# Kernel tuning notes

Measured on AMD Instinct MI355X. Metric: run time of the kernel, lower is better.

The kernel has to match this reference:

```python
import jax, jax.numpy as jnp
import numpy as np

B = 256      # batch
ZD = 128     # z_dim
HIN = 128    # H_inputs
H = 512      # hidden
HT = 32      # H_t
N = 16384    # num nodes
RW = 16      # rw_len
TEMP = 1.0
P_DROP = 0.2
EPS_C = 0.1  # constraints epsilon


def setup_inputs() -> dict:
    key = jax.random.key(0)
    ks = jax.random.split(key, 20)
    def w(k, shape, fan):
        return (jax.random.normal(k, shape, jnp.float32) / np.float32(np.sqrt(fan)))
    z = lambda n: jnp.zeros((n,), jnp.float32)
    u = jax.random.uniform(ks[14], (RW, B, N), jnp.float32)
    return {
        "latent": jax.random.normal(ks[0], (B, ZD + 1), jnp.float32),
        "inputs0": jnp.zeros((B, HIN), jnp.float32),
        "Wc": w(ks[1], (ZD, ZD + 1), ZD + 1), "bc": z(ZD),
        "Ws": w(ks[2], (H, ZD), ZD), "bs": z(H),
        "Wh": w(ks[3], (H, H), H), "bh": z(H),
        "Wcc": w(ks[4], (H, H), H), "bcc": z(H),
        "W_ih": w(ks[5], (4 * H, HIN), HIN), "b_ih": z(4 * H),
        "W_hh": w(ks[6], (4 * H, H), H), "b_hh": z(4 * H),
        "W_up": w(ks[7], (N, H), H), "b_up": z(N),
        "W_down": w(ks[8], (HIN, N), N),
        "Wt_down": w(ks[9], (HT, H), H), "bt_down": z(HT),
        "Wt_pred": w(ks[10], (1, HT), HT),
        "Wt_up": w(ks[11], (HT, 1), 1), "bt_up": z(HT),
        "W_vt": w(ks[12], (HIN, HIN + HT), HIN + HT),
        "W_prob": w(ks[13], (1, HIN), HIN),
        # pre-sampled Gumbel noise per step (torch.rand -> gumbel)
        "gumbel": -jnp.log(-jnp.log(u + 1e-20) + 1e-20),
        # uniforms for dropout masks in TimeDecoder (forced train mode)
        "drop_u": jax.random.uniform(ks[15], (RW, B, HT), jnp.float32),
    }


def reference(latent, inputs0, Wc, bc, Ws, bs, Wh, bh, Wcc, bcc,
              W_ih, b_ih, W_hh, b_hh, W_up, b_up, W_down,
              Wt_down, bt_down, Wt_pred, Wt_up, bt_up, W_vt, W_prob,
              gumbel, drop_u):
    # induced=True path: compress latent, init (h, c)
    lat = jnp.tanh(latent @ Wc.T + bc)               # [B, ZD]
    s = jnp.tanh(lat @ Ws.T + bs)                    # [B, H]
    h0 = jnp.tanh(s @ Wh.T + bh)
    c0 = jnp.tanh(s @ Wcc.T + bcc)
    keep = 1.0 - P_DROP

    def step(carry, xs):
        x, h, c, last_t = carry
        g, du = xs
        # torch LSTMCell: gate order i, f, g, o
        gates = x @ W_ih.T + b_ih + h @ W_hh.T + b_hh  # [B, 4H]
        i, f, gg, o = jnp.split(gates, 4, axis=1)
        c2 = jax.nn.sigmoid(f) * c + jax.nn.sigmoid(i) * jnp.tanh(gg)
        h2 = jax.nn.sigmoid(o) * jnp.tanh(c2)
        # node logits + gumbel-softmax sample
        p = h2 @ W_up.T + b_up                         # [B, N]
        v = jax.nn.softmax((p + g) / TEMP, axis=1)
        Hg = v @ W_down.T                              # [B, HIN]
        # TimeDecoder (dropout always in train mode)
        td = jnp.tanh(h2 @ Wt_down.T + bt_down)        # [B, HT]
        td = td * (du < keep).astype(td.dtype) / keep
        t = jnp.minimum(td @ Wt_pred.T, 1.0)           # [B, 1]
        # constraints(t, last_t)
        mn = jnp.min(t)
        t = jnp.where(mn < EPS_C, t - mn, t)
        mx = jnp.max(t)
        t = jnp.where(mx > 1.0, t / mx, t)
        t = jnp.clip(t, last_t, 1.0)
        Ht = t @ Wt_up.T + bt_up                       # [B, HT]
        x2 = jnp.concatenate([Hg, Ht], axis=1) @ W_vt.T  # [B, HIN]
        return (x2, h2, c2, t), (v, t)

    last_t0 = jnp.zeros((latent.shape[0], 1), latent.dtype)
    (xf, _, _, _), (rw, ts) = jax.lax.scan(step, (inputs0, h0, c0, last_t0), (gumbel, drop_u))
    rw = jnp.transpose(rw, (1, 0, 2))   # [B, RW, N]
    ts = jnp.transpose(ts, (1, 0, 2))   # [B, RW, 1]
    prob = xf @ W_prob.T                # [B, 1]
    return rw, ts, prob
```

## Files before the change

kernel.cpp:

```cpp
#include <hip/hip_runtime.h>

typedef float  __attribute__((ext_vector_type(4))) f32x4;
typedef int    __attribute__((ext_vector_type(4))) i32x4;
typedef unsigned short u16;
typedef unsigned long long u64;

#define B    256
#define H    512
#define HIN  128
#define N    16384
#define RW   16
#define HT   32
#define KC2  672
#define RWN  262144
#define TS_OFF   67108864
#define PROB_OFF 67112960

__device__ __forceinline__ u16 f2bf(float f) {
  unsigned u = __builtin_bit_cast(unsigned, f);
  u += 0x7FFFu + ((u >> 16) & 1u);
  return (u16)(u >> 16);
}
__device__ __forceinline__ float bf2f(u16 v) {
  return __builtin_bit_cast(float, ((unsigned)v) << 16);
}
__device__ __forceinline__ float sigm(float x) { return 1.0f / (1.0f + expf(-x)); }

__device__ __forceinline__ void mfma(f32x4& d, i32x4 a, i32x4 b) {
  asm volatile("v_mfma_f32_16x16x32_bf16 %0, %1, %2, %0" : "+v"(d) : "v"(a), "v"(b));
}
__device__ __forceinline__ void mfma_n(f32x4& d, i32x4 a, i32x4 b) {
  asm volatile("s_nop 1\n\tv_mfma_f32_16x16x32_bf16 %0, %1, %2, %0" : "+v"(d) : "v"(a), "v"(b));
}
__device__ __forceinline__ void fence_acc(f32x4& v) {
  asm volatile("s_nop 7\n\ts_nop 7" : "+v"(v));
}

__global__ __launch_bounds__(256) void k_prep(
    const float* __restrict__ W_up, const float* __restrict__ W_down,
    const float* __restrict__ W_hh, const float* __restrict__ Wt_down,
    const float* __restrict__ b_ih, const float* __restrict__ b_hh,
    const float* __restrict__ Wh, const float* __restrict__ Wcc,
    const float* __restrict__ W_ih, const float* __restrict__ W_vt,
    const float* __restrict__ inputs0, const float* __restrict__ W_prob,
    u16* __restrict__ Wup_b, u16* __restrict__ Wdn_b, u16* __restrict__ Wfull,
    u16* __restrict__ Wtd_b, u16* __restrict__ Whc_b,
    float* __restrict__ bcomb, float* __restrict__ tstep, float* __restrict__ rowLs,
    float* __restrict__ g0add, float* __restrict__ wpc)
{
  const int idx0 = blockIdx.x * 256 + threadIdx.x;
  const int stride = gridDim.x * 256;
  for (int i = idx0; i < N * H; i += stride) Wup_b[i] = f2bf(W_up[i]);
  for (int i = idx0; i < HIN * N; i += stride) Wdn_b[i] = f2bf(W_down[i]);
  for (int i = idx0; i < 4 * H * H; i += stride) {
    int j = i >> 9, k = i & 511;
    Wfull[j * KC2 + 160 + k] = f2bf(W_hh[i]);
  }
  for (int i = idx0; i < HT * H; i += stride) Wtd_b[i] = f2bf(Wt_down[i]);
  for (int i = idx0; i < 2 * H * H; i += stride) {
    int j = i >> 9, k = i & 511;
    Whc_b[i] = f2bf(j < H ? Wh[j * H + k] : Wcc[(j - H) * H + k]);
  }
  for (int i = idx0; i < 4 * H; i += stride) bcomb[i] = b_ih[i] + b_hh[i];
  for (int i = idx0; i < B; i += stride) tstep[i] = 0.0f;
  for (int i = idx0; i < 16 * B; i += stride) rowLs[i] = 0.0f;
  for (int i = idx0; i < 2048 * 160; i += stride) {
    int j = i / 160, m = i - j * 160;
    float a = 0.0f;
    for (int c = 0; c < HIN; ++c) a += W_ih[j * HIN + c] * W_vt[c * 160 + m];
    Wfull[j * KC2 + m] = f2bf(a);
  }
  for (int i = idx0; i < 256 * 2048; i += stride) {
    int b = i >> 11, j = i & 2047;
    float a = 0.0f;
    for (int k = 0; k < HIN; ++k) a += inputs0[b * HIN + k] * W_ih[j * HIN + k];
    g0add[i] = a;
  }
  for (int i = idx0; i < 160; i += stride) {
    float a = 0.0f;
    for (int k = 0; k < HIN; ++k) a += W_prob[k] * W_vt[k * 160 + i];
    wpc[i] = a;
  }
}

__global__ __launch_bounds__(256) void k_lat(
    const float* __restrict__ latent, const float* __restrict__ Wc,
    const float* __restrict__ bc, float* __restrict__ latbuf)
{
  int idx = blockIdx.x * 256 + threadIdx.x;
  int b = idx >> 7, i = idx & 127;
  float acc = bc[i];
  for (int k = 0; k < 129; ++k) acc += latent[b * 129 + k] * Wc[i * 129 + k];
  latbuf[idx] = tanhf(acc);
}

__global__ __launch_bounds__(256) void k_sinit(
    const float* __restrict__ latbuf, const float* __restrict__ Ws,
    const float* __restrict__ bs, u16* __restrict__ sinit_b)
{
  int idx = blockIdx.x * 256 + threadIdx.x;
  int b = idx >> 9, j = idx & 511;
  float acc = bs[j];
  for (int k = 0; k < HIN; ++k) acc += latbuf[b * HIN + k] * Ws[j * HIN + k];
  sinit_b[idx] = f2bf(tanhf(acc));
}

__global__ __launch_bounds__(256) void k_h0c0m(
    const u16* __restrict__ sinit_b, const u16* __restrict__ Whc_b,
    const float* __restrict__ bh, const float* __restrict__ bcc,
    float* __restrict__ cbuf, u16* __restrict__ h0out)
{
  const int rb = blockIdx.x >> 6, cb = blockIdx.x & 63;
  const int wave = threadIdx.x >> 6, lane = threadIdx.x & 63;
  const int lr = lane & 15, lk = lane >> 4;
  const int m0 = rb * 16, col0 = cb * 16;
  const u16* ab = sinit_b + (m0 + lr) * H + wave * 128 + 8 * lk;
  const u16* bb = Whc_b + (col0 + lr) * H + wave * 128 + 8 * lk;
  f32x4 acc[2] = {};
  mfma_n(acc[0], *(const i32x4*)(ab),      *(const i32x4*)(bb));
  mfma_n(acc[1], *(const i32x4*)(ab + 32), *(const i32x4*)(bb + 32));
  mfma(acc[0], *(const i32x4*)(ab + 64), *(const i32x4*)(bb + 64));
  mfma(acc[1], *(const i32x4*)(ab + 96), *(const i32x4*)(bb + 96));
  fence_acc(acc[0]); fence_acc(acc[1]);
  __shared__ float q[4][16][17];
  #pragma unroll
  for (int rr = 0; rr < 4; ++rr)
    q[wave][4 * lk + rr][lr] = acc[0][rr] + acc[1][rr];
  __syncthreads();
  const int r2 = threadIdx.x >> 4, jj = threadIdx.x & 15;
  float s = q[0][r2][jj] + q[1][r2][jj] + q[2][r2][jj] + q[3][r2][jj];
  int col = col0 + jj;
  if (col < H) h0out[(m0 + r2) * H + col] = f2bf(tanhf(s + bh[col]));
  else         cbuf[(m0 + r2) * H + col - H] = tanhf(s + bcc[col - H]);
}

__global__ __launch_bounds__(256) void k_lstm2(
    const u16* __restrict__ hprev, u16* __restrict__ hcur,
    const u16* __restrict__ Wfull, const float* __restrict__ bcomb,
    float* __restrict__ cbuf, const float* __restrict__ g0,
    const float* __restrict__ HgXprev, float* __restrict__ HgXcur,
    const float* __restrict__ rowLs, const float* __restrict__ t0buf,
    float* __restrict__ tstep, const float* __restrict__ Wt_up,
    const float* __restrict__ bt_up, float* __restrict__ out, int r)
{
  const int blk = blockIdx.x, tid = threadIdx.x;
  const int wave = tid >> 6, lane = tid & 63;
  const int lr = lane & 15, lk = lane >> 4;
  const int rb = blk & 15, cb = blk >> 4;
  const int m0 = rb * 16, j0 = cb * 16;
  const float* rowLprev = rowLs + (r - 1) * B;

  __shared__ u16 aT[16][168];
  __shared__ float q[4][16][17];
  __shared__ float redS[8];
  __shared__ float tl[256];

  HgXcur[blk * 512 + tid] = 0.0f;
  HgXcur[blk * 512 + 256 + tid] = 0.0f;

  float tv = 0.0f;
  if (r > 0) {
    tv = t0buf[tid];
    float v = tv;
    #pragma unroll
    for (int off = 1; off < 64; off <<= 1) v = fminf(v, __shfl_xor(v, off));
    if (lane == 0) redS[wave] = v;
  }
  __syncthreads();
  if (r > 0) {
    float mn = fminf(fminf(redS[0], redS[1]), fminf(redS[2], redS[3]));
    if (mn < 0.1f) tv -= mn;
    float v = tv;
    #pragma unroll
    for (int off = 1; off < 64; off <<= 1) v = fmaxf(v, __shfl_xor(v, off));
    if (lane == 0) redS[4 + wave] = v;
  }
  __syncthreads();
  if (r > 0) {
    float mx = fmaxf(fmaxf(redS[4], redS[5]), fmaxf(redS[6], redS[7]));
    if (mx > 1.0f) tv /= mx;
    tv = fminf(fmaxf(tv, tstep[(r - 1) * B + tid]), 1.0f);
    if (blk == 0) {
      tstep[r * B + tid] = tv;
      out[TS_OFF + tid * RW + (r - 1)] = tv;
    }
  }
  tl[tid] = tv;

  {
    const int row = tid >> 4, c8 = (tid & 15) * 8;
    if (r > 0) {
      const float* hp = HgXprev + (size_t)(m0 + row) * HIN + c8;
      f32x4 A0 = {}, A1 = {};
      #pragma unroll
      for (int x = 0; x < 8; ++x) {
        A0 += *(const f32x4*)(hp + (size_t)x * (B * HIN));
        A1 += *(const f32x4*)(hp + (size_t)x * (B * HIN) + 4);
      }
      float R = 1.0f / rowLprev[m0 + row];
      aT[row][c8 + 0] = f2bf(A0[0] * R); aT[row][c8 + 1] = f2bf(A0[1] * R);
      aT[row][c8 + 2] = f2bf(A0[2] * R); aT[row][c8 + 3] = f2bf(A0[3] * R);
      aT[row][c8 + 4] = f2bf(A1[0] * R); aT[row][c8 + 5] = f2bf(A1[1] * R);
      aT[row][c8 + 6] = f2bf(A1[2] * R); aT[row][c8 + 7] = f2bf(A1[3] * R);
    } else {
      #pragma unroll
      for (int e = 0; e < 8; ++e) aT[row][c8 + e] = 0;
    }
  }
  __syncthreads();

  for (int i2 = tid; i2 < 512; i2 += 256) {
    int row = i2 >> 5, j = i2 & 31;
    aT[row][128 + j] = (r > 0) ? f2bf(tl[m0 + row] * Wt_up[j] + bt_up[j]) : (u16)0;
  }
  __syncthreads();

  const int gcol = wave * H + j0 + lr;
  f32x4 acc[2] = {};
  const u16* brow = Wfull + (size_t)gcol * KC2 + 8 * lk;
  const u16* aL   = &aT[lr][8 * lk];
  const u16* arow = hprev + (m0 + lr) * H + 8 * lk;
  mfma_n(acc[0], *(const i32x4*)(aL),       *(const i32x4*)(brow));
  mfma_n(acc[1], *(const i32x4*)(aL + 32),  *(const i32x4*)(brow + 32));
  mfma(acc[0], *(const i32x4*)(aL + 64),  *(const i32x4*)(brow + 64));
  mfma(acc[1], *(const i32x4*)(aL + 96),  *(const i32x4*)(brow + 96));
  mfma(acc[0], *(const i32x4*)(aL + 128), *(const i32x4*)(brow + 128));
  #pragma unroll 4
  for (int i = 5; i < 21; ++i) {
    int kk = i * 32;
    mfma(acc[i & 1], *(const i32x4*)(arow + kk - 160), *(const i32x4*)(brow + kk));
  }
  fence_acc(acc[0]); fence_acc(acc[1]);
  float bias = bcomb[gcol];
  #pragma unroll
  for (int rr = 0; rr < 4; ++rr)
    q[wave][4 * lk + rr][lr] = acc[0][rr] + acc[1][rr] + bias;
  __syncthreads();
  const int r2 = tid >> 4, jj = tid & 15;
  const int b = m0 + r2, j = j0 + jj;
  float gi = q[0][r2][jj], gf = q[1][r2][jj], gg = q[2][r2][jj], go = q[3][r2][jj];
  if (r == 0) {
    const float* gp = g0 + b * 2048 + j;
    gi += gp[0]; gf += gp[512]; gg += gp[1024]; go += gp[1536];
  }
  float c  = cbuf[b * H + j];
  float c2 = sigm(gf) * c + sigm(gi) * tanhf(gg);
  float h2 = sigm(go) * tanhf(c2);
  cbuf[b * H + j] = c2;
  hcur[b * H + j] = f2bf(h2);
}

__global__ __launch_bounds__(256) void k_pgemm2(
    const u16* __restrict__ hb, const u16* __restrict__ Wup,
    const float* __restrict__ b_up, const float* __restrict__ gum,
    u16* __restrict__ eb, const u16* __restrict__ ebp,
    float* __restrict__ rowL, const float* __restrict__ rowLs,
    float* __restrict__ HgX, const u16* __restrict__ Wdn,
    const u16* __restrict__ Wtd, const float* __restrict__ bt_down,
    const float* __restrict__ Wt_pred, const float* __restrict__ du,
    float* __restrict__ t0, float* __restrict__ out, int r)
{
  const int blk = blockIdx.x;
  const int rb = blk >> 7, cb = blk & 127;
  const int wave = threadIdx.x >> 6, lane = threadIdx.x & 63;
  const int lr = lane & 15, lk = lane >> 4;
  const int m0 = rb * 32;
  const int n0 = cb * 128 + wave * 32;

  float gv[2][4][2], bup0 = b_up[n0 + lr], bup1 = b_up[n0 + 16 + lr];
  #pragma unroll
  for (int mi = 0; mi < 2; ++mi)
    #pragma unroll
    for (int rr = 0; rr < 4; ++rr) {
      int row = m0 + 16 * mi + 4 * lk + rr;
      gv[mi][rr][0] = gum[(size_t)row * N + n0 + lr];
      gv[mi][rr][1] = gum[(size_t)row * N + n0 + 16 + lr];
    }

  if (r > 0) {
    const float* rowLprev = rowLs + (r - 1) * B;
    #pragma unroll
    for (int uu = 0; uu < 4; ++uu) {
      int flat = (blk * 1024 + uu * 256 + (int)threadIdx.x) * 4;
      int row = flat >> 14;
      float Rv = 1.0f / rowLprev[row];
      u64 ev = *(const u64*)(ebp + flat);
      f32x4 o;
      o[0] = bf2f((u16)ev) * Rv;
      o[1] = bf2f((u16)(ev >> 16)) * Rv;
      o[2] = bf2f((u16)(ev >> 32)) * Rv;
      o[3] = bf2f((u16)(ev >> 48)) * Rv;
      *(f32x4*)(out + (size_t)row * RWN + (size_t)(r - 1) * N + (flat & (N - 1))) = o;
    }
  }

  f32x4 acc[2][2] = {};
  const u16* a0 = hb + (m0 + lr) * H + 8 * lk;
  const u16* a1 = a0 + 16 * H;
  const u16* b0 = Wup + (size_t)(n0 + lr) * H + 8 * lk;
  const u16* b1 = b0 + 16 * H;
  {
    i32x4 af0 = *(const i32x4*)(a0);
    i32x4 af1 = *(const i32x4*)(a1);
    i32x4 bf0 = *(const i32x4*)(b0);
    i32x4 bf1 = *(const i32x4*)(b1);
    mfma_n(acc[0][0], af0, bf0); mfma_n(acc[0][1], af0, bf1);
    mfma_n(acc[1][0], af1, bf0); mfma_n(acc[1][1], af1, bf1);
  }
  #pragma unroll 3
  for (int kk = 32; kk < H; kk += 32) {
    i32x4 af0 = *(const i32x4*)(a0 + kk);
    i32x4 af1 = *(const i32x4*)(a1 + kk);
    i32x4 bf0 = *(const i32x4*)(b0 + kk);
    i32x4 bf1 = *(const i32x4*)(b1 + kk);
    mfma(acc[0][0], af0, bf0); mfma(acc[0][1], af0, bf1);
    mfma(acc[1][0], af1, bf0); mfma(acc[1][1], af1, bf1);
  }
  #pragma unroll
  for (int mi = 0; mi < 2; ++mi) { fence_acc(acc[mi][0]); fence_acc(acc[mi][1]); }

  __shared__ u16 eLb[32][136];
  __shared__ float sL[4][32];
  #pragma unroll
  for (int mi = 0; mi < 2; ++mi)
    #pragma unroll
    for (int rr = 0; rr < 4; ++rr) {
      int rl = 16 * mi + 4 * lk + rr;
      int row = m0 + rl;
      u16* sp = eb + (size_t)row * N + n0 + lr;
      float v0 = acc[mi][0][rr] + bup0 + gv[mi][rr][0];
      float v1 = acc[mi][1][rr] + bup1 + gv[mi][rr][1];
      float e0 = expf(fminf(v0, 80.0f));
      float e1 = expf(fminf(v1, 80.0f));
      u16 p0 = f2bf(e0), p1 = f2bf(e1);
      sp[0] = p0; sp[16] = p1;
      eLb[rl][wave * 32 + lr] = p0;
      eLb[rl][wave * 32 + 16 + lr] = p1;
      float par = e0 + e1;
      #pragma unroll
      for (int off = 1; off < 16; off <<= 1) par += __shfl_xor(par, off);
      if (lr == 0) sL[wave][rl] = par;
    }
  __syncthreads();
  if (threadIdx.x < 32)
    atomicAdd(rowL + m0 + threadIdx.x,
              sL[0][threadIdx.x] + sL[1][threadIdx.x] + sL[2][threadIdx.x] + sL[3][threadIdx.x]);

  const int nb = cb * 128;
  float* hgs = HgX + (size_t)(blk & 7) * (B * HIN);
  f32x4 acc2[2][2] = {};
  #pragma unroll
  for (int kk2 = 0; kk2 < 4; ++kk2) {
    i32x4 af0 = *(const i32x4*)(&eLb[lr][kk2 * 32 + 8 * lk]);
    i32x4 af1 = *(const i32x4*)(&eLb[16 + lr][kk2 * 32 + 8 * lk]);
    i32x4 bf0 = *(const i32x4*)(Wdn + (size_t)(wave * 32 + lr) * N + nb + kk2 * 32 + 8 * lk);
    i32x4 bf1 = *(const i32x4*)(Wdn + (size_t)(wave * 32 + 16 + lr) * N + nb + kk2 * 32 + 8 * lk);
    mfma(acc2[0][0], af0, bf0); mfma(acc2[0][1], af0, bf1);
    mfma(acc2[1][0], af1, bf0); mfma(acc2[1][1], af1, bf1);
  }
  #pragma unroll
  for (int mi2 = 0; mi2 < 2; ++mi2) { fence_acc(acc2[mi2][0]); fence_acc(acc2[mi2][1]); }
  #pragma unroll
  for (int mi2 = 0; mi2 < 2; ++mi2)
    #pragma unroll
    for (int ni = 0; ni < 2; ++ni)
      #pragma unroll
      for (int rr = 0; rr < 4; ++rr)
        atomicAdd(hgs + (m0 + 16 * mi2 + 4 * lk + rr) * HIN + wave * 32 + 16 * ni + lr,
                  acc2[mi2][ni][rr]);

  if (cb == 0 && wave < 2) {
    f32x4 acc3[2] = {};
    const u16* at = hb + (m0 + wave * 16 + lr) * H + 8 * lk;
    {
      i32x4 af = *(const i32x4*)(at);
      mfma_n(acc3[0], af, *(const i32x4*)(Wtd + lr * H + 8 * lk));
      mfma_n(acc3[1], af, *(const i32x4*)(Wtd + (16 + lr) * H + 8 * lk));
    }
    for (int kk = 32; kk < H; kk += 32) {
      i32x4 af = *(const i32x4*)(at + kk);
      mfma(acc3[0], af, *(const i32x4*)(Wtd + lr * H + kk + 8 * lk));
      mfma(acc3[1], af, *(const i32x4*)(Wtd + (16 + lr) * H + kk + 8 * lk));
    }
    fence_acc(acc3[0]); fence_acc(acc3[1]);
    float wp0 = Wt_pred[lr],  wp1 = Wt_pred[16 + lr];
    float bt0 = bt_down[lr],  bt1 = bt_down[16 + lr];
    #pragma unroll
    for (int rr = 0; rr < 4; ++rr) {
      int row = m0 + wave * 16 + 4 * lk + rr;
      float td0 = tanhf(acc3[0][rr] + bt0);
      float td1 = tanhf(acc3[1][rr] + bt1);
      td0 = (du[row * HT + lr]      < 0.8f) ? td0 * 1.25f : 0.0f;
      td1 = (du[row * HT + 16 + lr] < 0.8f) ? td1 * 1.25f : 0.0f;
      float part = td0 * wp0 + td1 * wp1;
      #pragma unroll
      for (int off = 1; off < 16; off <<= 1) part += __shfl_xor(part, off);
      if (lr == 0) t0[row] = fminf(part, 1.0f);
    }
  }
}

__global__ __launch_bounds__(256) void k_tail(
    float* __restrict__ out, const u16* __restrict__ eb15,
    const float* __restrict__ rowLs, const float* __restrict__ t0buf,
    float* __restrict__ tstep, const float* __restrict__ HgX15,
    const float* __restrict__ Wt_up, const float* __restrict__ bt_up,
    const float* __restrict__ wpc)
{
  const int blk = blockIdx.x, tid = threadIdx.x;
  const float* rowL15 = rowLs + 15 * B;
  if (blk < 1024) {
    #pragma unroll
    for (int uu = 0; uu < 4; ++uu) {
      int flat = (blk * 1024 + uu * 256 + tid) * 4;
      int row = flat >> 14;
      float Rv = 1.0f / rowL15[row];
      u64 ev = *(const u64*)(eb15 + flat);
      f32x4 o;
      o[0] = bf2f((u16)ev) * Rv;
      o[1] = bf2f((u16)(ev >> 16)) * Rv;
      o[2] = bf2f((u16)(ev >> 32)) * Rv;
      o[3] = bf2f((u16)(ev >> 48)) * Rv;
      *(f32x4*)(out + (size_t)row * RWN + (size_t)15 * N + (flat & (N - 1))) = o;
    }
  }
  if (blk == 0 || blk == 1024) {
    const int wave = tid >> 6, lane = tid & 63;
    __shared__ float redS[8];
    float tv = t0buf[tid];
    float v = tv;
    #pragma unroll
    for (int off = 1; off < 64; off <<= 1) v = fminf(v, __shfl_xor(v, off));
    if (lane == 0) redS[wave] = v;
    __syncthreads();
    float mn = fminf(fminf(redS[0], redS[1]), fminf(redS[2], redS[3]));
    if (mn < 0.1f) tv -= mn;
    v = tv;
    #pragma unroll
    for (int off = 1; off < 64; off <<= 1) v = fmaxf(v, __shfl_xor(v, off));
    if (lane == 0) redS[4 + wave] = v;
    __syncthreads();
    float mx = fmaxf(fmaxf(redS[4], redS[5]), fmaxf(redS[6], redS[7]));
    if (mx > 1.0f) tv /= mx;
    tv = fminf(fmaxf(tv, tstep[15 * B + tid]), 1.0f);
    if (blk == 0) out[TS_OFF + tid * RW + 15] = tv;
    else {
      float R = 1.0f / rowL15[tid];
      float acc = 0.0f;
      for (int m = 0; m < HIN; ++m) {
        float hg = 0.0f;
        #pragma unroll
        for (int x = 0; x < 8; ++x) hg += HgX15[(size_t)x * (B * HIN) + tid * HIN + m];
        acc += hg * R * wpc[m];
      }
      for (int j = 0; j < HT; ++j) acc += (tv * Wt_up[j] + bt_up[j]) * wpc[HIN + j];
      out[PROB_OFF + tid] = acc;
    }
  }
}

extern "C" void kernel_launch(void* const* d_in, const int* in_sizes, int n_in,
                              void* d_out, int out_size, void* d_ws, size_t ws_size,
                              hipStream_t stream) {
  (void)in_sizes; (void)n_in; (void)out_size; (void)ws_size;
  const float* latent  = (const float*)d_in[0];
  const float* inputs0 = (const float*)d_in[1];
  const float* Wc      = (const float*)d_in[2];
  const float* bc      = (const float*)d_in[3];
  const float* Ws      = (const float*)d_in[4];
  const float* bs      = (const float*)d_in[5];
  const float* Wh      = (const float*)d_in[6];
  const float* bh      = (const float*)d_in[7];
  const float* Wcc     = (const float*)d_in[8];
  const float* bcc     = (const float*)d_in[9];
  const float* W_ih    = (const float*)d_in[10];
  const float* b_ih    = (const float*)d_in[11];
  const float* W_hh    = (const float*)d_in[12];
  const float* b_hh    = (const float*)d_in[13];
  const float* W_up    = (const float*)d_in[14];
  const float* b_up    = (const float*)d_in[15];
  const float* W_down  = (const float*)d_in[16];
  const float* Wt_down = (const float*)d_in[17];
  const float* bt_down = (const float*)d_in[18];
  const float* Wt_pred = (const float*)d_in[19];
  const float* Wt_up   = (const float*)d_in[20];
  const float* bt_up   = (const float*)d_in[21];
  const float* W_vt    = (const float*)d_in[22];
  const float* W_prob  = (const float*)d_in[23];
  const float* gumbel  = (const float*)d_in[24];
  const float* drop_u  = (const float*)d_in[25];
  float* out = (float*)d_out;

  char* p = (char*)d_ws;
  auto alloc = [&](size_t bytes) { char* r = p; p += (bytes + 255) & ~(size_t)255; return r; };
  u16*   Wup_b  = (u16*)  alloc((size_t)N * H * 2);
  u16*   Wdn_b  = (u16*)  alloc((size_t)HIN * N * 2);
  u16*   Wfull_b= (u16*)  alloc((size_t)4 * H * KC2 * 2);
  u16*   Wtd_b  = (u16*)  alloc((size_t)HT * H * 2);
  u16*   Whc_b  = (u16*)  alloc((size_t)2 * H * H * 2);
  float* bcomb  = (float*)alloc(4 * H * 4);
  u16*   hbuf0  = (u16*)  alloc((size_t)B * H * 2);
  u16*   hbuf1  = (u16*)  alloc((size_t)B * H * 2);
  float* cbuf   = (float*)alloc((size_t)B * H * 4);
  u16*   sinit_b= (u16*)  alloc((size_t)B * H * 2);
  float* latbuf = (float*)alloc((size_t)B * HIN * 4);
  float* rowLs  = (float*)alloc((size_t)16 * B * 4);
  float* t0buf  = (float*)alloc(B * 4);
  float* tstep  = (float*)alloc((size_t)17 * B * 4);
  float* HgX0   = (float*)alloc((size_t)8 * B * HIN * 4);
  float* HgX1   = (float*)alloc((size_t)8 * B * HIN * 4);
  float* g0add  = (float*)alloc((size_t)B * 4 * H * 4);
  float* wpc    = (float*)alloc(160 * 4);
  u16*   ebuf0  = (u16*)  alloc((size_t)B * N * 2);
  u16*   ebuf1  = (u16*)  alloc((size_t)B * N * 2);

  k_prep<<<2048, 256, 0, stream>>>(W_up, W_down, W_hh, Wt_down, b_ih, b_hh, Wh, Wcc,
                                   W_ih, W_vt, inputs0, W_prob,
                                   Wup_b, Wdn_b, Wfull_b, Wtd_b, Whc_b, bcomb,
                                   tstep, rowLs, g0add, wpc);
  k_lat  <<<128, 256, 0, stream>>>(latent, Wc, bc, latbuf);
  k_sinit<<<512, 256, 0, stream>>>(latbuf, Ws, bs, sinit_b);
  k_h0c0m<<<1024, 256, 0, stream>>>(sinit_b, Whc_b, bh, bcc, cbuf, hbuf1);

  for (int r = 0; r < 16; ++r) {
    u16* hprev = (r & 1) ? hbuf0 : hbuf1;
    u16* hcur  = (r & 1) ? hbuf1 : hbuf0;
    u16* eb    = (r & 1) ? ebuf1 : ebuf0;
    u16* ebp   = (r & 1) ? ebuf0 : ebuf1;
    float* HgXc = (r & 1) ? HgX1 : HgX0;
    float* HgXp = (r & 1) ? HgX0 : HgX1;
    k_lstm2<<<512, 256, 0, stream>>>(hprev, hcur, Wfull_b, bcomb, cbuf, g0add,
                                     HgXp, HgXc, rowLs, t0buf, tstep,
                                     Wt_up, bt_up, out, r);
    k_pgemm2<<<1024, 256, 0, stream>>>(hcur, Wup_b, b_up, gumbel + (size_t)r * B * N,
                                       eb, ebp, rowLs + r * B, rowLs, HgXc, Wdn_b,
                                       Wtd_b, bt_down, Wt_pred,
                                       drop_u + (size_t)r * B * HT, t0buf, out, r);
  }
  k_tail<<<1025, 256, 0, stream>>>(out, ebuf1, rowLs, t0buf, tstep, HgX1,
                                   Wt_up, bt_up, wpc);
}
```

Measured before the change: 1.354 ms.

## Fuse recurrent steps into one persistent cooperative kernel with grid barriers

Replaces the 32 per-step kernel launches plus the tail with one cooperative persistent kernel that alternates the LSTM phase and the projection/softmax phase, separated by a hierarchical atomic grid barrier. Per-step buffers (h, t, Hg) are indexed by step instead of double-buffered, and Hg is accumulated directly into one buffer rather than 8 partial slices. The softmax normalization now writes unnormalized exp values in fp32 to the output and rescales them in place during the next step's LSTM phase, using otherwise idle blocks. The aim is to remove launch gaps and the bf16 staging buffer, at the cost of barrier spin overhead, more atomic contention on Hg, and reliance on cooperative launch with a multi-launch fallback.

```diff
diff --git a/kernel.cpp b/kernel.cpp
--- a/kernel.cpp
+++ b/kernel.cpp
@@ -3,7 +3,7 @@
 typedef float  __attribute__((ext_vector_type(4))) f32x4;
 typedef int    __attribute__((ext_vector_type(4))) i32x4;
 typedef unsigned short u16;
-typedef unsigned long long u64;
+typedef unsigned int u32;
 
 #define B    256
 #define H    512
@@ -15,15 +15,15 @@
 #define RWN  262144
 #define TS_OFF   67108864
 #define PROB_OFF 67112960
+#define NBLK 1024
+#define NGRP 32
+#define GRPSZ 32
 
 __device__ __forceinline__ u16 f2bf(float f) {
   unsigned u = __builtin_bit_cast(unsigned, f);
   u += 0x7FFFu + ((u >> 16) & 1u);
   return (u16)(u >> 16);
 }
-__device__ __forceinline__ float bf2f(u16 v) {
-  return __builtin_bit_cast(float, ((unsigned)v) << 16);
-}
 __device__ __forceinline__ float sigm(float x) { return 1.0f / (1.0f + expf(-x)); }
 
 __device__ __forceinline__ void mfma(f32x4& d, i32x4 a, i32x4 b) {
@@ -34,6 +34,326 @@
 }
 __device__ __forceinline__ void fence_acc(f32x4& v) {
   asm volatile("s_nop 7\n\ts_nop 7" : "+v"(v));
+}
+__device__ __forceinline__ void dstoref(float* p, float v) {
+  __hip_atomic_store(p, v, __ATOMIC_RELAXED, __HIP_MEMORY_SCOPE_AGENT);
+}
+__device__ __forceinline__ void dstoreu(u32* p, u32 v) {
+  __hip_atomic_store(p, v, __ATOMIC_RELAXED, __HIP_MEMORY_SCOPE_AGENT);
+}
+
+__device__ __forceinline__ void gsync(u32* bar, int gen) {
+  __syncthreads();
+  if (threadIdx.x == 0) {
+    const int g = blockIdx.x & (NGRP - 1);
+    u32 t = __hip_atomic_fetch_add(bar + g * 32, 1u, __ATOMIC_RELAXED, __HIP_MEMORY_SCOPE_AGENT);
+    if ((t % GRPSZ) == GRPSZ - 1) {
+      __hip_atomic_fetch_add(bar + 1024, 1u, __ATOMIC_RELAXED, __HIP_MEMORY_SCOPE_AGENT);
+      while (__hip_atomic_load(bar + 1024, __ATOMIC_RELAXED, __HIP_MEMORY_SCOPE_AGENT)
+             < (u32)(gen * NGRP))
+        __builtin_amdgcn_s_sleep(4);
+      __hip_atomic_store(bar + 2048 + g * 32, (u32)gen, __ATOMIC_RELAXED, __HIP_MEMORY_SCOPE_AGENT);
+    } else {
+      while (__hip_atomic_load(bar + 2048 + g * 32, __ATOMIC_RELAXED, __HIP_MEMORY_SCOPE_AGENT)
+             < (u32)gen)
+        __builtin_amdgcn_s_sleep(4);
+    }
+  }
+  __syncthreads();
+}
+
+struct GArgs {
+  const u16 *Wfull, *Wup, *Wdn, *Wtd, *h0buf;
+  const float *bcomb, *g0add, *b_up, *gumbel, *du, *Wt_pred, *bt_down,
+              *Wt_up, *bt_up, *wpc;
+  u16 *hbufs;
+  float *cbuf, *Hgfs, *rowLs, *t0bufs, *tstep, *out;
+};
+
+struct SmL {
+  u16 aT[16][168];
+  float q[4][16][17];
+  float redS[8];
+  float tl[256];
+};
+struct SmP {
+  u16 eLb[32][136];
+  float sL[4][32];
+};
+union Smem { SmL l; SmP p; };
+
+__device__ void phase_L(const GArgs& A, Smem* sm, int r) {
+  const int blk = blockIdx.x, tid = threadIdx.x;
+  if (blk >= 512) {
+    if (r > 0) {
+      const float* rowLp = A.rowLs + (r - 1) * B;
+      const int vb = blk - 512;
+      #pragma unroll
+      for (int uu = 0; uu < 8; ++uu) {
+        int flat = (vb * 2048 + uu * 256 + tid) * 4;
+        int row = flat >> 14;
+        float Rv = 1.0f / rowLp[row];
+        float* op = A.out + (size_t)row * RWN + (size_t)(r - 1) * N + (flat & (N - 1));
+        f32x4 o = *(f32x4*)op;
+        o[0] *= Rv; o[1] *= Rv; o[2] *= Rv; o[3] *= Rv;
+        *(f32x4*)op = o;
+      }
+    }
+    return;
+  }
+  const int wave = tid >> 6, lane = tid & 63;
+  const int lr = lane & 15, lk = lane >> 4;
+  const int rb = blk & 15, cb = blk >> 4;
+  const int m0 = rb * 16, j0 = cb * 16;
+  const bool tc = (r > 0) && (r < 16 || blk == 0);
+
+  float tv = 0.0f;
+  if (tc) {
+    tv = A.t0bufs[(size_t)(r - 1) * B + tid];
+    float v = tv;
+    #pragma unroll
+    for (int off = 1; off < 64; off <<= 1) v = fminf(v, __shfl_xor(v, off));
+    if (lane == 0) sm->l.redS[wave] = v;
+  }
+  __syncthreads();
+  if (tc) {
+    float mn = fminf(fminf(sm->l.redS[0], sm->l.redS[1]), fminf(sm->l.redS[2], sm->l.redS[3]));
+    if (mn < 0.1f) tv -= mn;
+    float v = tv;
+    #pragma unroll
+    for (int off = 1; off < 64; off <<= 1) v = fmaxf(v, __shfl_xor(v, off));
+    if (lane == 0) sm->l.redS[4 + wave] = v;
+  }
+  __syncthreads();
+  if (tc) {
+    float mx = fmaxf(fmaxf(sm->l.redS[4], sm->l.redS[5]), fmaxf(sm->l.redS[6], sm->l.redS[7]));
+    if (mx > 1.0f) tv /= mx;
+    tv = fminf(fmaxf(tv, A.tstep[(size_t)(r - 1) * B + tid]), 1.0f);
+    if (blk == 0) {
+      dstoref(A.tstep + (size_t)r * B + tid, tv);
+      A.out[TS_OFF + tid * RW + (r - 1)] = tv;
+    }
+  }
+  sm->l.tl[tid] = tv;
+
+  if (r == 16) {
+    if (blk == 0) {
+      float R = 1.0f / A.rowLs[15 * B + tid];
+      const float* hg = A.Hgfs + (size_t)15 * B * HIN + tid * HIN;
+      float acc = 0.0f;
+      #pragma unroll 8
+      for (int m = 0; m < HIN; ++m) acc += hg[m] * A.wpc[m];
+      acc *= R;
+      for (int j = 0; j < HT; ++j) acc += (tv * A.Wt_up[j] + A.bt_up[j]) * A.wpc[HIN + j];
+      A.out[PROB_OFF + tid] = acc;
+    }
+    return;
+  }
+
+  {
+    const int row = tid >> 4, c8 = (tid & 15) * 8;
+    if (r > 0) {
+      const float* hp = A.Hgfs + (size_t)(r - 1) * B * HIN + (m0 + row) * HIN + c8;
+      f32x4 x0 = *(const f32x4*)hp;
+      f32x4 x1 = *(const f32x4*)(hp + 4);
+      float R = 1.0f / A.rowLs[(size_t)(r - 1) * B + m0 + row];
+      sm->l.aT[row][c8 + 0] = f2bf(x0[0] * R); sm->l.aT[row][c8 + 1] = f2bf(x0[1] * R);
+      sm->l.aT[row][c8 + 2] = f2bf(x0[2] * R); sm->l.aT[row][c8 + 3] = f2bf(x0[3] * R);
+      sm->l.aT[row][c8 + 4] = f2bf(x1[0] * R); sm->l.aT[row][c8 + 5] = f2bf(x1[1] * R);
+      sm->l.aT[row][c8 + 6] = f2bf(x1[2] * R); sm->l.aT[row][c8 + 7] = f2bf(x1[3] * R);
+    } else {
+      #pragma unroll
+      for (int e = 0; e < 8; ++e) sm->l.aT[row][c8 + e] = 0;
+    }
+  }
+  __syncthreads();
+  for (int i2 = tid; i2 < 512; i2 += 256) {
+    int row = i2 >> 5, j = i2 & 31;
+    sm->l.aT[row][128 + j] = (r > 0) ? f2bf(sm->l.tl[m0 + row] * A.Wt_up[j] + A.bt_up[j]) : (u16)0;
+  }
+  __syncthreads();
+
+  const u16* hprev = (r == 0) ? A.h0buf : A.hbufs + (size_t)(r - 1) * B * H;
+  const int gcol = wave * H + j0 + lr;
+  f32x4 acc[2] = {};
+  const u16* brow = A.Wfull + (size_t)gcol * KC2 + 8 * lk;
+  const u16* aL   = &sm->l.aT[lr][8 * lk];
+  const u16* arow = hprev + (m0 + lr) * H + 8 * lk;
+  mfma_n(acc[0], *(const i32x4*)(aL),       *(const i32x4*)(brow));
+  mfma_n(acc[1], *(const i32x4*)(aL + 32),  *(const i32x4*)(brow + 32));
+  mfma(acc[0], *(const i32x4*)(aL + 64),  *(const i32x4*)(brow + 64));
+  mfma(acc[1], *(const i32x4*)(aL + 96),  *(const i32x4*)(brow + 96));
+  mfma(acc[0], *(const i32x4*)(aL + 128), *(const i32x4*)(brow + 128));
+  #pragma unroll 4
+  for (int i = 5; i < 21; ++i) {
+    int kk = i * 32;
+    mfma(acc[i & 1], *(const i32x4*)(arow + kk - 160), *(const i32x4*)(brow + kk));
+  }
+  fence_acc(acc[0]); fence_acc(acc[1]);
+  float bias = A.bcomb[gcol];
+  #pragma unroll
+  for (int rr = 0; rr < 4; ++rr)
+    sm->l.q[wave][4 * lk + rr][lr] = acc[0][rr] + acc[1][rr] + bias;
+  __syncthreads();
+  const int r2 = tid >> 4, jj = tid & 15;
+  const int b = m0 + r2, j = j0 + jj;
+  float gi = sm->l.q[0][r2][jj], gf = sm->l.q[1][r2][jj];
+  float gg = sm->l.q[2][r2][jj], go = sm->l.q[3][r2][jj];
+  if (r == 0) {
+    const float* gp = A.g0add + b * 2048 + j;
+    gi += gp[0]; gf += gp[512]; gg += gp[1024]; go += gp[1536];
+  }
+  float c  = A.cbuf[b * H + j];
+  float c2 = sigm(gf) * c + sigm(gi) * tanhf(gg);
+  float h2 = sigm(go) * tanhf(c2);
+  A.cbuf[b * H + j] = c2;
+  u32 hv = f2bf(h2);
+  u32 other = __shfl_xor(hv, 1);
+  if (!(tid & 1))
+    dstoreu((u32*)(A.hbufs + (size_t)r * B * H + b * H + j), hv | (other << 16));
+}
+
+__device__ void phase_P(const GArgs& A, Smem* sm, int r) {
+  const int blk = blockIdx.x, tid = threadIdx.x;
+  const int rb = blk >> 7, cb = blk & 127;
+  const int wave = tid >> 6, lane = tid & 63;
+  const int lr = lane & 15, lk = lane >> 4;
+  const int m0 = rb * 32;
+  const int n0 = cb * 128 + wave * 32;
+  const u16* hb = A.hbufs + (size_t)r * B * H;
+  const float* gum = A.gumbel + (size_t)r * B * N;
+  float* rowL = A.rowLs + (size_t)r * B;
+  float* HgfAcc = A.Hgfs + (size_t)r * B * HIN;
+
+  float gv[2][4][2], bup0 = A.b_up[n0 + lr], bup1 = A.b_up[n0 + 16 + lr];
+  #pragma unroll
+  for (int mi = 0; mi < 2; ++mi)
+    #pragma unroll
+    for (int rr = 0; rr < 4; ++rr) {
+      int row = m0 + 16 * mi + 4 * lk + rr;
+      gv[mi][rr][0] = gum[(size_t)row * N + n0 + lr];
+      gv[mi][rr][1] = gum[(size_t)row * N + n0 + 16 + lr];
+    }
+
+  f32x4 acc[2][2] = {};
+  const u16* a0 = hb + (m0 + lr) * H + 8 * lk;
+  const u16* a1 = a0 + 16 * H;
+  const u16* b0 = A.Wup + (size_t)(n0 + lr) * H + 8 * lk;
+  const u16* b1 = b0 + 16 * H;
+  {
+    i32x4 af0 = *(const i32x4*)(a0);
+    i32x4 af1 = *(const i32x4*)(a1);
+    i32x4 bf0 = *(const i32x4*)(b0);
+    i32x4 bf1 = *(const i32x4*)(b1);
+    mfma_n(acc[0][0], af0, bf0); mfma_n(acc[0][1], af0, bf1);
+    mfma_n(acc[1][0], af1, bf0); mfma_n(acc[1][1], af1, bf1);
+  }
+  #pragma unroll 3
+  for (int kk = 32; kk < H; kk += 32) {
+    i32x4 af0 = *(const i32x4*)(a0 + kk);
+    i32x4 af1 = *(const i32x4*)(a1 + kk);
+    i32x4 bf0 = *(const i32x4*)(b0 + kk);
+    i32x4 bf1 = *(const i32x4*)(b1 + kk);
+    mfma(acc[0][0], af0, bf0); mfma(acc[0][1], af0, bf1);
+    mfma(acc[1][0], af1, bf0); mfma(acc[1][1], af1, bf1);
+  }
+  #pragma unroll
+  for (int mi = 0; mi < 2; ++mi) { fence_acc(acc[mi][0]); fence_acc(acc[mi][1]); }
+
+  #pragma unroll
+  for (int mi = 0; mi < 2; ++mi)
+    #pragma unroll
+    for (int rr = 0; rr < 4; ++rr) {
+      int rl = 16 * mi + 4 * lk + rr;
+      int row = m0 + rl;
+      float* sp = A.out + (size_t)row * RWN + (size_t)r * N + n0 + lr;
+      float v0 = acc[mi][0][rr] + bup0 + gv[mi][rr][0];
+      float v1 = acc[mi][1][rr] + bup1 + gv[mi][rr][1];
+      float e0 = expf(fminf(v0, 80.0f));
+      float e1 = expf(fminf(v1, 80.0f));
+      dstoref(sp, e0); dstoref(sp + 16, e1);
+      sm->p.eLb[rl][wave * 32 + lr] = f2bf(e0);
+      sm->p.eLb[rl][wave * 32 + 16 + lr] = f2bf(e1);
+      float par = e0 + e1;
+      #pragma unroll
+      for (int off = 1; off < 16; off <<= 1) par += __shfl_xor(par, off);
+      if (lr == 0) sm->p.sL[wave][rl] = par;
+    }
+  __syncthreads();
+  if (tid < 32)
+    atomicAdd(rowL + m0 + tid,
+              sm->p.sL[0][tid] + sm->p.sL[1][tid] + sm->p.sL[2][tid] + sm->p.sL[3][tid]);
+
+  const int nb = cb * 128;
+  f32x4 acc2[2][2] = {};
+  #pragma unroll
+  for (int kk2 = 0; kk2 < 4; ++kk2) {
+    i32x4 af0 = *(const i32x4*)(&sm->p.eLb[lr][kk2 * 32 + 8 * lk]);
+    i32x4 af1 = *(const i32x4*)(&sm->p.eLb[16 + lr][kk2 * 32 + 8 * lk]);
+    i32x4 bf0 = *(const i32x4*)(A.Wdn + (size_t)(wave * 32 + lr) * N + nb + kk2 * 32 + 8 * lk);
+    i32x4 bf1 = *(const i32x4*)(A.Wdn + (size_t)(wave * 32 + 16 + lr) * N + nb + kk2 * 32 + 8 * lk);
+    mfma(acc2[0][0], af0, bf0); mfma(acc2[0][1], af0, bf1);
+    mfma(acc2[1][0], af1, bf0); mfma(acc2[1][1], af1, bf1);
+  }
+  #pragma unroll
+  for (int mi2 = 0; mi2 < 2; ++mi2) { fence_acc(acc2[mi2][0]); fence_acc(acc2[mi2][1]); }
+  #pragma unroll
+  for (int mi2 = 0; mi2 < 2; ++mi2)
+    #pragma unroll
+    for (int ni = 0; ni < 2; ++ni)
+      #pragma unroll
+      for (int rr = 0; rr < 4; ++rr)
+        atomicAdd(HgfAcc + (m0 + 16 * mi2 + 4 * lk + rr) * HIN + wave * 32 + 16 * ni + lr,
+                  acc2[mi2][ni][rr]);
+
+  if (cb == 0 && wave < 2) {
+    const float* du = A.du + (size_t)r * B * HT;
+    f32x4 acc3[2] = {};
+    const u16* at = hb + (m0 + wave * 16 + lr) * H + 8 * lk;
+    {
+      i32x4 af = *(const i32x4*)(at);
+      mfma_n(acc3[0], af, *(const i32x4*)(A.Wtd + lr * H + 8 * lk));
+      mfma_n(acc3[1], af, *(const i32x4*)(A.Wtd + (16 + lr) * H + 8 * lk));
+    }
+    for (int kk = 32; kk < H; kk += 32) {
+      i32x4 af = *(const i32x4*)(at + kk);
+      mfma(acc3[0], af, *(const i32x4*)(A.Wtd + lr * H + kk + 8 * lk));
+      mfma(acc3[1], af, *(const i32x4*)(A.Wtd + (16 + lr) * H + kk + 8 * lk));
+    }
+    fence_acc(acc3[0]); fence_acc(acc3[1]);
+    float wp0 = A.Wt_pred[lr],  wp1 = A.Wt_pred[16 + lr];
+    float bt0 = A.bt_down[lr],  bt1 = A.bt_down[16 + lr];
+    #pragma unroll
+    for (int rr = 0; rr < 4; ++rr) {
+      int row = m0 + wave * 16 + 4 * lk + rr;
+      float td0 = tanhf(acc3[0][rr] + bt0);
+      float td1 = tanhf(acc3[1][rr] + bt1);
+      td0 = (du[row * HT + lr]      < 0.8f) ? td0 * 1.25f : 0.0f;
+      td1 = (du[row * HT + 16 + lr] < 0.8f) ? td1 * 1.25f : 0.0f;
+      float part = td0 * wp0 + td1 * wp1;
+      #pragma unroll
+      for (int off = 1; off < 16; off <<= 1) part += __shfl_xor(part, off);
+      if (lr == 0) dstoref(A.t0bufs + (size_t)r * B + row, fminf(part, 1.0f));
+    }
+  }
+}
+
+__global__ __launch_bounds__(256, 4) void k_step(GArgs A, u32* bar) {
+  __shared__ Smem sm;
+  int gen = 0;
+  for (int r = 0; r < 16; ++r) {
+    phase_L(A, &sm, r);
+    gsync(bar, ++gen);
+    phase_P(A, &sm, r);
+    gsync(bar, ++gen);
+  }
+  phase_L(A, &sm, 16);
+}
+__global__ __launch_bounds__(256, 4) void k_phL(GArgs A, int r) {
+  __shared__ Smem sm; phase_L(A, &sm, r);
+}
+__global__ __launch_bounds__(256, 4) void k_phP(GArgs A, int r) {
+  __shared__ Smem sm; phase_P(A, &sm, r);
 }
 
 __global__ __launch_bounds__(256) void k_prep(
@@ -46,7 +366,8 @@
     u16* __restrict__ Wup_b, u16* __restrict__ Wdn_b, u16* __restrict__ Wfull,
     u16* __restrict__ Wtd_b, u16* __restrict__ Whc_b,
     float* __restrict__ bcomb, float* __restrict__ tstep, float* __restrict__ rowLs,
-    float* __restrict__ g0add, float* __restrict__ wpc)
+    float* __restrict__ g0add, float* __restrict__ wpc,
+    float* __restrict__ Hgfs, u32* __restrict__ bar)
 {
   const int idx0 = blockIdx.x * 256 + threadIdx.x;
   const int stride = gridDim.x * 256;
@@ -64,6 +385,8 @@
   for (int i = idx0; i < 4 * H; i += stride) bcomb[i] = b_ih[i] + b_hh[i];
   for (int i = idx0; i < B; i += stride) tstep[i] = 0.0f;
   for (int i = idx0; i < 16 * B; i += stride) rowLs[i] = 0.0f;
+  for (int i = idx0; i < 16 * B * HIN; i += stride) Hgfs[i] = 0.0f;
+  for (int i = idx0; i < 4096; i += stride) bar[i] = 0u;
   for (int i = idx0; i < 2048 * 160; i += stride) {
     int j = i / 160, m = i - j * 160;
     float a = 0.0f;
@@ -132,331 +455,6 @@
   int col = col0 + jj;
   if (col < H) h0out[(m0 + r2) * H + col] = f2bf(tanhf(s + bh[col]));
   else         cbuf[(m0 + r2) * H + col - H] = tanhf(s + bcc[col - H]);
-}
-
-__global__ __launch_bounds__(256) void k_lstm2(
-    const u16* __restrict__ hprev, u16* __restrict__ hcur,
-    const u16* __restrict__ Wfull, const float* __restrict__ bcomb,
-    float* __restrict__ cbuf, const float* __restrict__ g0,
-    const float* __restrict__ HgXprev, float* __restrict__ HgXcur,
-    const float* __restrict__ rowLs, const float* __restrict__ t0buf,
-    float* __restrict__ tstep, const float* __restrict__ Wt_up,
-    const float* __restrict__ bt_up, float* __restrict__ out, int r)
-{
-  const int blk = blockIdx.x, tid = threadIdx.x;
-  const int wave = tid >> 6, lane = tid & 63;
-  const int lr = lane & 15, lk = lane >> 4;
-  const int rb = blk & 15, cb = blk >> 4;
-  const int m0 = rb * 16, j0 = cb * 16;
-  const float* rowLprev = rowLs + (r - 1) * B;
-
-  __shared__ u16 aT[16][168];
-  __shared__ float q[4][16][17];
-  __shared__ float redS[8];
-  __shared__ float tl[256];
-
-  HgXcur[blk * 512 + tid] = 0.0f;
-  HgXcur[blk * 512 + 256 + tid] = 0.0f;
-
-  float tv = 0.0f;
-  if (r > 0) {
-    tv = t0buf[tid];
-    float v = tv;
-    #pragma unroll
-    for (int off = 1; off < 64; off <<= 1) v = fminf(v, __shfl_xor(v, off));
-    if (lane == 0) redS[wave] = v;
-  }
-  __syncthreads();
-  if (r > 0) {
-    float mn = fminf(fminf(redS[0], redS[1]), fminf(redS[2], redS[3]));
-    if (mn < 0.1f) tv -= mn;
-    float v = tv;
-    #pragma unroll
-    for (int off = 1; off < 64; off <<= 1) v = fmaxf(v, __shfl_xor(v, off));
-    if (lane == 0) redS[4 + wave] = v;
-  }
-  __syncthreads();
-  if (r > 0) {
-    float mx = fmaxf(fmaxf(redS[4], redS[5]), fmaxf(redS[6], redS[7]));
-    if (mx > 1.0f) tv /= mx;
-    tv = fminf(fmaxf(tv, tstep[(r - 1) * B + tid]), 1.0f);
-    if (blk == 0) {
-      tstep[r * B + tid] = tv;
-      out[TS_OFF + tid * RW + (r - 1)] = tv;
-    }
-  }
-  tl[tid] = tv;
-
-  {
-    const int row = tid >> 4, c8 = (tid & 15) * 8;
-    if (r > 0) {
-      const float* hp = HgXprev + (size_t)(m0 + row) * HIN + c8;
-      f32x4 A0 = {}, A1 = {};
-      #pragma unroll
-      for (int x = 0; x < 8; ++x) {
-        A0 += *(const f32x4*)(hp + (size_t)x * (B * HIN));
-        A1 += *(const f32x4*)(hp + (size_t)x * (B * HIN) + 4);
-      }
-      float R = 1.0f / rowLprev[m0 + row];
-      aT[row][c8 + 0] = f2bf(A0[0] * R); aT[row][c8 + 1] = f2bf(A0[1] * R);
-      aT[row][c8 + 2] = f2bf(A0[2] * R); aT[row][c8 + 3] = f2bf(A0[3] * R);
-      aT[row][c8 + 4] = f2bf(A1[0] * R); aT[row][c8 + 5] = f2bf(A1[1] * R);
-      aT[row][c8 + 6] = f2bf(A1[2] * R); aT[row][c8 + 7] = f2bf(A1[3] * R);
-    } else {
-      #pragma unroll
-      for (int e = 0; e < 8; ++e) aT[row][c8 + e] = 0;
-    }
-  }
-  __syncthreads();
-
-  for (int i2 = tid; i2 < 512; i2 += 256) {
-    int row = i2 >> 5, j = i2 & 31;
-    aT[row][128 + j] = (r > 0) ? f2bf(tl[m0 + row] * Wt_up[j] + bt_up[j]) : (u16)0;
-  }
-  __syncthreads();
-
-  const int gcol = wave * H + j0 + lr;
-  f32x4 acc[2] = {};
-  const u16* brow = Wfull + (size_t)gcol * KC2 + 8 * lk;
-  const u16* aL   = &aT[lr][8 * lk];
-  const u16* arow = hprev + (m0 + lr) * H + 8 * lk;
-  mfma_n(acc[0], *(const i32x4*)(aL),       *(const i32x4*)(brow));
-  mfma_n(acc[1], *(const i32x4*)(aL + 32),  *(const i32x4*)(brow + 32));
-  mfma(acc[0], *(const i32x4*)(aL + 64),  *(const i32x4*)(brow + 64));
-  mfma(acc[1], *(const i32x4*)(aL + 96),  *(const i32x4*)(brow + 96));
-  mfma(acc[0], *(const i32x4*)(aL + 128), *(const i32x4*)(brow + 128));
-  #pragma unroll 4
-  for (int i = 5; i < 21; ++i) {
-    int kk = i * 32;
-    mfma(acc[i & 1], *(const i32x4*)(arow + kk - 160), *(const i32x4*)(brow + kk));
-  }
-  fence_acc(acc[0]); fence_acc(acc[1]);
-  float bias = bcomb[gcol];
-  #pragma unroll
-  for (int rr = 0; rr < 4; ++rr)
-    q[wave][4 * lk + rr][lr] = acc[0][rr] + acc[1][rr] + bias;
-  __syncthreads();
-  const int r2 = tid >> 4, jj = tid & 15;
-  const int b = m0 + r2, j = j0 + jj;
-  float gi = q[0][r2][jj], gf = q[1][r2][jj], gg = q[2][r2][jj], go = q[3][r2][jj];
-  if (r == 0) {
-    const float* gp = g0 + b * 2048 + j;
-    gi += gp[0]; gf += gp[512]; gg += gp[1024]; go += gp[1536];
-  }
-  float c  = cbuf[b * H + j];
-  float c2 = sigm(gf) * c + sigm(gi) * tanhf(gg);
-  float h2 = sigm(go) * tanhf(c2);
-  cbuf[b * H + j] = c2;
-  hcur[b * H + j] = f2bf(h2);
-}
-
-__global__ __launch_bounds__(256) void k_pgemm2(
-    const u16* __restrict__ hb, const u16* __restrict__ Wup,
-    const float* __restrict__ b_up, const float* __restrict__ gum,
-    u16* __restrict__ eb, const u16* __restrict__ ebp,
-    float* __restrict__ rowL, const float* __restrict__ rowLs,
-    float* __restrict__ HgX, const u16* __restrict__ Wdn,
-    const u16* __restrict__ Wtd, const float* __restrict__ bt_down,
-    const float* __restrict__ Wt_pred, const float* __restrict__ du,
-    float* __restrict__ t0, float* __restrict__ out, int r)
-{
-  const int blk = blockIdx.x;
-  const int rb = blk >> 7, cb = blk & 127;
-  const int wave = threadIdx.x >> 6, lane = threadIdx.x & 63;
-  const int lr = lane & 15, lk = lane >> 4;
-  const int m0 = rb * 32;
-  const int n0 = cb * 128 + wave * 32;
-
-  float gv[2][4][2], bup0 = b_up[n0 + lr], bup1 = b_up[n0 + 16 + lr];
-  #pragma unroll
-  for (int mi = 0; mi < 2; ++mi)
-    #pragma unroll
-    for (int rr = 0; rr < 4; ++rr) {
-      int row = m0 + 16 * mi + 4 * lk + rr;
-      gv[mi][rr][0] = gum[(size_t)row * N + n0 + lr];
-      gv[mi][rr][1] = gum[(size_t)row * N + n0 + 16 + lr];
-    }
-
-  if (r > 0) {
-    const float* rowLprev = rowLs + (r - 1) * B;
-    #pragma unroll
-    for (int uu = 0; uu < 4; ++uu) {
-      int flat = (blk * 1024 + uu * 256 + (int)threadIdx.x) * 4;
-      int row = flat >> 14;
-      float Rv = 1.0f / rowLprev[row];
-      u64 ev = *(const u64*)(ebp + flat);
-      f32x4 o;
-      o[0] = bf2f((u16)ev) * Rv;
-      o[1] = bf2f((u16)(ev >> 16)) * Rv;
-      o[2] = bf2f((u16)(ev >> 32)) * Rv;
-      o[3] = bf2f((u16)(ev >> 48)) * Rv;
-      *(f32x4*)(out + (size_t)row * RWN + (size_t)(r - 1) * N + (flat & (N - 1))) = o;
-    }
-  }
-
-  f32x4 acc[2][2] = {};
-  const u16* a0 = hb + (m0 + lr) * H + 8 * lk;
-  const u16* a1 = a0 + 16 * H;
-  const u16* b0 = Wup + (size_t)(n0 + lr) * H + 8 * lk;
-  const u16* b1 = b0 + 16 * H;
-  {
-    i32x4 af0 = *(const i32x4*)(a0);
-    i32x4 af1 = *(const i32x4*)(a1);
-    i32x4 bf0 = *(const i32x4*)(b0);
-    i32x4 bf1 = *(const i32x4*)(b1);
-    mfma_n(acc[0][0], af0, bf0); mfma_n(acc[0][1], af0, bf1);
-    mfma_n(acc[1][0], af1, bf0); mfma_n(acc[1][1], af1, bf1);
-  }
-  #pragma unroll 3
-  for (int kk = 32; kk < H; kk += 32) {
-    i32x4 af0 = *(const i32x4*)(a0 + kk);
-    i32x4 af1 = *(const i32x4*)(a1 + kk);
-    i32x4 bf0 = *(const i32x4*)(b0 + kk);
-    i32x4 bf1 = *(const i32x4*)(b1 + kk);
-    mfma(acc[0][0], af0, bf0); mfma(acc[0][1], af0, bf1);
-    mfma(acc[1][0], af1, bf0); mfma(acc[1][1], af1, bf1);
-  }
-  #pragma unroll
-  for (int mi = 0; mi < 2; ++mi) { fence_acc(acc[mi][0]); fence_acc(acc[mi][1]); }
-
-  __shared__ u16 eLb[32][136];
-  __shared__ float sL[4][32];
-  #pragma unroll
-  for (int mi = 0; mi < 2; ++mi)
-    #pragma unroll
-    for (int rr = 0; rr < 4; ++rr) {
-      int rl = 16 * mi + 4 * lk + rr;
-      int row = m0 + rl;
-      u16* sp = eb + (size_t)row * N + n0 + lr;
-      float v0 = acc[mi][0][rr] + bup0 + gv[mi][rr][0];
-      float v1 = acc[mi][1][rr] + bup1 + gv[mi][rr][1];
-      float e0 = expf(fminf(v0, 80.0f));
-      float e1 = expf(fminf(v1, 80.0f));
-      u16 p0 = f2bf(e0), p1 = f2bf(e1);
-      sp[0] = p0; sp[16] = p1;
-      eLb[rl][wave * 32 + lr] = p0;
-      eLb[rl][wave * 32 + 16 + lr] = p1;
-      float par = e0 + e1;
-      #pragma unroll
-      for (int off = 1; off < 16; off <<= 1) par += __shfl_xor(par, off);
-      if (lr == 0) sL[wave][rl] = par;
-    }
-  __syncthreads();
-  if (threadIdx.x < 32)
-    atomicAdd(rowL + m0 + threadIdx.x,
-              sL[0][threadIdx.x] + sL[1][threadIdx.x] + sL[2][threadIdx.x] + sL[3][threadIdx.x]);
-
-  const int nb = cb * 128;
-  float* hgs = HgX + (size_t)(blk & 7) * (B * HIN);
-  f32x4 acc2[2][2] = {};
-  #pragma unroll
-  for (int kk2 = 0; kk2 < 4; ++kk2) {
-    i32x4 af0 = *(const i32x4*)(&eLb[lr][kk2 * 32 + 8 * lk]);
-    i32x4 af1 = *(const i32x4*)(&eLb[16 + lr][kk2 * 32 + 8 * lk]);
-    i32x4 bf0 = *(const i32x4*)(Wdn + (size_t)(wave * 32 + lr) * N + nb + kk2 * 32 + 8 * lk);
-    i32x4 bf1 = *(const i32x4*)(Wdn + (size_t)(wave * 32 + 16 + lr) * N + nb + kk2 * 32 + 8 * lk);
-    mfma(acc2[0][0], af0, bf0); mfma(acc2[0][1], af0, bf1);
-    mfma(acc2[1][0], af1, bf0); mfma(acc2[1][1], af1, bf1);
-  }
-  #pragma unroll
-  for (int mi2 = 0; mi2 < 2; ++mi2) { fence_acc(acc2[mi2][0]); fence_acc(acc2[mi2][1]); }
-  #pragma unroll
-  for (int mi2 = 0; mi2 < 2; ++mi2)
-    #pragma unroll
-    for (int ni = 0; ni < 2; ++ni)
-      #pragma unroll
-      for (int rr = 0; rr < 4; ++rr)
-        atomicAdd(hgs + (m0 + 16 * mi2 + 4 * lk + rr) * HIN + wave * 32 + 16 * ni + lr,
-                  acc2[mi2][ni][rr]);
-
-  if (cb == 0 && wave < 2) {
-    f32x4 acc3[2] = {};
-    const u16* at = hb + (m0 + wave * 16 + lr) * H + 8 * lk;
-    {
-      i32x4 af = *(const i32x4*)(at);
-      mfma_n(acc3[0], af, *(const i32x4*)(Wtd + lr * H + 8 * lk));
-      mfma_n(acc3[1], af, *(const i32x4*)(Wtd + (16 + lr) * H + 8 * lk));
-    }
-    for (int kk = 32; kk < H; kk += 32) {
-      i32x4 af = *(const i32x4*)(at + kk);
-      mfma(acc3[0], af, *(const i32x4*)(Wtd + lr * H + kk + 8 * lk));
-      mfma(acc3[1], af, *(const i32x4*)(Wtd + (16 + lr) * H + kk + 8 * lk));
-    }
-    fence_acc(acc3[0]); fence_acc(acc3[1]);
-    float wp0 = Wt_pred[lr],  wp1 = Wt_pred[16 + lr];
-    float bt0 = bt_down[lr],  bt1 = bt_down[16 + lr];
-    #pragma unroll
-    for (int rr = 0; rr < 4; ++rr) {
-      int row = m0 + wave * 16 + 4 * lk + rr;
-      float td0 = tanhf(acc3[0][rr] + bt0);
-      float td1 = tanhf(acc3[1][rr] + bt1);
-      td0 = (du[row * HT + lr]      < 0.8f) ? td0 * 1.25f : 0.0f;
-      td1 = (du[row * HT + 16 + lr] < 0.8f) ? td1 * 1.25f : 0.0f;
-      float part = td0 * wp0 + td1 * wp1;
-      #pragma unroll
-      for (int off = 1; off < 16; off <<= 1) part += __shfl_xor(part, off);
-      if (lr == 0) t0[row] = fminf(part, 1.0f);
-    }
-  }
-}
-
-__global__ __launch_bounds__(256) void k_tail(
-    float* __restrict__ out, const u16* __restrict__ eb15,
-    const float* __restrict__ rowLs, const float* __restrict__ t0buf,
-    float* __restrict__ tstep, const float* __restrict__ HgX15,
-    const float* __restrict__ Wt_up, const float* __restrict__ bt_up,
-    const float* __restrict__ wpc)
-{
-  const int blk = blockIdx.x, tid = threadIdx.x;
-  const float* rowL15 = rowLs + 15 * B;
-  if (blk < 1024) {
-    #pragma unroll
-    for (int uu = 0; uu < 4; ++uu) {
-      int flat = (blk * 1024 + uu * 256 + tid) * 4;
-      int row = flat >> 14;
-      float Rv = 1.0f / rowL15[row];
-      u64 ev = *(const u64*)(eb15 + flat);
-      f32x4 o;
-      o[0] = bf2f((u16)ev) * Rv;
-      o[1] = bf2f((u16)(ev >> 16)) * Rv;
-      o[2] = bf2f((u16)(ev >> 32)) * Rv;
-      o[3] = bf2f((u16)(ev >> 48)) * Rv;
-      *(f32x4*)(out + (size_t)row * RWN + (size_t)15 * N + (flat & (N - 1))) = o;
-    }
-  }
-  if (blk == 0 || blk == 1024) {
-    const int wave = tid >> 6, lane = tid & 63;
-    __shared__ float redS[8];
-    float tv = t0buf[tid];
-    float v = tv;
-    #pragma unroll
-    for (int off = 1; off < 64; off <<= 1) v = fminf(v, __shfl_xor(v, off));
-    if (lane == 0) redS[wave] = v;
-    __syncthreads();
-    float mn = fminf(fminf(redS[0], redS[1]), fminf(redS[2], redS[3]));
-    if (mn < 0.1f) tv -= mn;
-    v = tv;
-    #pragma unroll
-    for (int off = 1; off < 64; off <<= 1) v = fmaxf(v, __shfl_xor(v, off));
-    if (lane == 0) redS[4 + wave] = v;
-    __syncthreads();
-    float mx = fmaxf(fmaxf(redS[4], redS[5]), fmaxf(redS[6], redS[7]));
-    if (mx > 1.0f) tv /= mx;
-    tv = fminf(fmaxf(tv, tstep[15 * B + tid]), 1.0f);
-    if (blk == 0) out[TS_OFF + tid * RW + 15] = tv;
-    else {
-      float R = 1.0f / rowL15[tid];
-      float acc = 0.0f;
-      for (int m = 0; m < HIN; ++m) {
-        float hg = 0.0f;
-        #pragma unroll
-        for (int x = 0; x < 8; ++x) hg += HgX15[(size_t)x * (B * HIN) + tid * HIN + m];
-        acc += hg * R * wpc[m];
-      }
-      for (int j = 0; j < HT; ++j) acc += (tv * Wt_up[j] + bt_up[j]) * wpc[HIN + j];
-      out[PROB_OFF + tid] = acc;
-    }
-  }
 }
 
 extern "C" void kernel_launch(void* const* d_in, const int* in_sizes, int n_in,
@@ -499,44 +497,44 @@
   u16*   Wtd_b  = (u16*)  alloc((size_t)HT * H * 2);
   u16*   Whc_b  = (u16*)  alloc((size_t)2 * H * H * 2);
   float* bcomb  = (float*)alloc(4 * H * 4);
-  u16*   hbuf0  = (u16*)  alloc((size_t)B * H * 2);
-  u16*   hbuf1  = (u16*)  alloc((size_t)B * H * 2);
+  u16*   hbufs  = (u16*)  alloc((size_t)16 * B * H * 2);
+  u16*   h0buf  = (u16*)  alloc((size_t)B * H * 2);
   float* cbuf   = (float*)alloc((size_t)B * H * 4);
   u16*   sinit_b= (u16*)  alloc((size_t)B * H * 2);
   float* latbuf = (float*)alloc((size_t)B * HIN * 4);
   float* rowLs  = (float*)alloc((size_t)16 * B * 4);
-  float* t0buf  = (float*)alloc(B * 4);
+  float* t0bufs = (float*)alloc((size_t)16 * B * 4);
   float* tstep  = (float*)alloc((size_t)17 * B * 4);
-  float* HgX0   = (float*)alloc((size_t)8 * B * HIN * 4);
-  float* HgX1   = (float*)alloc((size_t)8 * B * HIN * 4);
+  float* Hgfs   = (float*)alloc((size_t)16 * B * HIN * 4);
   float* g0add  = (float*)alloc((size_t)B * 4 * H * 4);
   float* wpc    = (float*)alloc(160 * 4);
-  u16*   ebuf0  = (u16*)  alloc((size_t)B * N * 2);
-  u16*   ebuf1  = (u16*)  alloc((size_t)B * N * 2);
+  u32*   bar    = (u32*)  alloc(4096 * 4);
 
   k_prep<<<2048, 256, 0, stream>>>(W_up, W_down, W_hh, Wt_down, b_ih, b_hh, Wh, Wcc,
                                    W_ih, W_vt, inputs0, W_prob,
                                    Wup_b, Wdn_b, Wfull_b, Wtd_b, Whc_b, bcomb,
-                                   tstep, rowLs, g0add, wpc);
+                                   tstep, rowLs, g0add, wpc, Hgfs, bar);
   k_lat  <<<128, 256, 0, stream>>>(latent, Wc, bc, latbuf);
   k_sinit<<<512, 256, 0, stream>>>(latbuf, Ws, bs, sinit_b);
-  k_h0c0m<<<1024, 256, 0, stream>>>(sinit_b, Whc_b, bh, bcc, cbuf, hbuf1);
-
-  for (int r = 0; r < 16; ++r) {
-    u16* hprev = (r & 1) ? hbuf0 : hbuf1;
-    u16* hcur  = (r & 1) ? hbuf1 : hbuf0;
-    u16* eb    = (r & 1) ? ebuf1 : ebuf0;
-    u16* ebp   = (r & 1) ? ebuf0 : ebuf1;
-    float* HgXc = (r & 1) ? HgX1 : HgX0;
-    float* HgXp = (r & 1) ? HgX0 : HgX1;
-    k_lstm2<<<512, 256, 0, stream>>>(hprev, hcur, Wfull_b, bcomb, cbuf, g0add,
-                                     HgXp, HgXc, rowLs, t0buf, tstep,
-                                     Wt_up, bt_up, out, r);
-    k_pgemm2<<<1024, 256, 0, stream>>>(hcur, Wup_b, b_up, gumbel + (size_t)r * B * N,
-                                       eb, ebp, rowLs + r * B, rowLs, HgXc, Wdn_b,
-                                       Wtd_b, bt_down, Wt_pred,
-                                       drop_u + (size_t)r * B * HT, t0buf, out, r);
-  }
-  k_tail<<<1025, 256, 0, stream>>>(out, ebuf1, rowLs, t0buf, tstep, HgX1,
-                                   Wt_up, bt_up, wpc);
-}
+  k_h0c0m<<<1024, 256, 0, stream>>>(sinit_b, Whc_b, bh, bcc, cbuf, h0buf);
+
+  GArgs A;
+  A.Wfull = Wfull_b; A.Wup = Wup_b; A.Wdn = Wdn_b; A.Wtd = Wtd_b; A.h0buf = h0buf;
+  A.bcomb = bcomb; A.g0add = g0add; A.b_up = b_up; A.gumbel = gumbel; A.du = drop_u;
+  A.Wt_pred = Wt_pred; A.bt_down = bt_down; A.Wt_up = Wt_up; A.bt_up = bt_up; A.wpc = wpc;
+  A.hbufs = hbufs; A.cbuf = cbuf; A.Hgfs = Hgfs; A.rowLs = rowLs;
+  A.t0bufs = t0bufs; A.tstep = tstep; A.out = out;
+
+  void* kargs[] = { (void*)&A, (void*)&bar };
+  hipError_t ce = hipLaunchCooperativeKernel(
+      reinterpret_cast<const void*>(&k_step), dim3(NBLK), dim3(256), kargs, 0, stream);
+
+  if (ce != hipSuccess) {
+    (void)hipGetLastError();
+    for (int r = 0; r < 16; ++r) {
+      k_phL<<<NBLK, 256, 0, stream>>>(A, r);
+      k_phP<<<NBLK, 256, 0, stream>>>(A, r);
+    }
+    k_phL<<<NBLK, 256, 0, stream>>>(A, 16);
+  }
+}
```

Measured after the change: 1.569 ms. 1.16x slower.
